# Kernel optimization log

Hardware: AMD Instinct MI355X
Metric: run time of the kernel (lower is better)

## Reference

```python
import math
import jax, jax.numpy as jnp
import numpy as np

D_MODEL = 768
NUM_HEADS = 12
NUM_KV_HEADS = 12
FEATURE_DIM = 16
HEAD_DIM = D_MODEL // NUM_KV_HEADS  # 64
EPS = 1e-12
R2 = math.sqrt(2.0)
RD = math.sqrt(FEATURE_DIM)      # sqrt(d)
RRD = math.sqrt(RD)              # d**0.25


def taylor_exp(x):
    """2nd-order Taylor feature map. x: [b,h,l,f] -> [b,h,l,1+f+f^2]."""
    b, h, l, f = x.shape
    x2 = (x[..., :, None] * x[..., None, :]).reshape(b, h, l, f * f) / R2
    ones = jnp.ones((b, h, l, 1), dtype=x.dtype)
    return jnp.concatenate([ones, x / RRD, x2 / RD], axis=-1)


def setup_inputs() -> dict:
    key = jax.random.key(0)
    k0, k1, k2, k3, k4 = jax.random.split(key, 5)
    B, L = 1, 512
    hidden_states = jax.random.normal(k0, (B, L, D_MODEL), dtype=jnp.float32)
    s = 0.02
    Wq = jax.random.normal(k1, (FEATURE_DIM * NUM_HEADS, D_MODEL), dtype=jnp.float32) * s
    Wk = jax.random.normal(k2, (FEATURE_DIM * NUM_KV_HEADS, D_MODEL), dtype=jnp.float32) * s
    Wv = jax.random.normal(k3, (NUM_KV_HEADS * HEAD_DIM, D_MODEL), dtype=jnp.float32) * s
    Wo = jax.random.normal(k4, (D_MODEL, NUM_HEADS * HEAD_DIM), dtype=jnp.float32) * s
    return {"hidden_states": hidden_states, "Wq": Wq, "Wk": Wk, "Wv": Wv, "Wo": Wo}


def reference(hidden_states, Wq, Wk, Wv, Wo):
    b, l, _ = hidden_states.shape
    # projections (nn.Linear, no bias): x @ W.T
    q = (hidden_states @ Wq.T).reshape(b, l, NUM_HEADS, FEATURE_DIM).transpose(0, 2, 1, 3)
    k = (hidden_states @ Wk.T).reshape(b, l, NUM_KV_HEADS, FEATURE_DIM).transpose(0, 2, 1, 3)
    v = (hidden_states @ Wv.T).reshape(b, l, NUM_KV_HEADS, HEAD_DIM).transpose(0, 2, 1, 3)
    q = taylor_exp(q)  # [b,h,l,D], D = 273
    k = taylor_exp(k)
    # causal linear attention: state S_t = sum_{s<=t} v_s phi(k_s)^T
    kv = k[..., None, :] * v[..., :, None]          # [b,h,l,d,D]
    kv = jnp.cumsum(kv, axis=2)
    num = jnp.einsum('bhlD,bhldD->bhld', q, kv)     # [b,h,l,d]
    den = jnp.einsum('bhlD,bhlD->bhl', q, jnp.cumsum(k, axis=2)) + EPS
    y = num / den[..., None]
    y = y.transpose(0, 2, 1, 3).reshape(b, l, NUM_HEADS * HEAD_DIM)
    return y @ Wo.T
```

## Files before the change

### kernel.cpp

```cpp
#include <hip/hip_runtime.h>

typedef short bf16x8 __attribute__((ext_vector_type(8)));
typedef float f32x4 __attribute__((ext_vector_type(4)));

__device__ __forceinline__ unsigned short f2bf(float f) {
  union { float f; unsigned int u; } v; v.f = f;
  unsigned int r = v.u + 0x7FFFu + ((v.u >> 16) & 1u);
  return (unsigned short)(r >> 16);
}

__global__ __launch_bounds__(256) void prep(
    const float* __restrict__ hs, const float* __restrict__ Wq,
    const float* __restrict__ Wk, const float* __restrict__ Wv,
    const float* __restrict__ Wo, unsigned short* __restrict__ hsb,
    unsigned short* __restrict__ Wqkvb, unsigned short* __restrict__ Wob,
    float* __restrict__ numAcc) {
  int b = blockIdx.x;
  const float* src; unsigned short* dst; int base;
  if (b < 384)       { src = hs; dst = hsb;            base = b * 1024; }
  else if (b < 528)  { src = Wq; dst = Wqkvb;          base = (b - 384) * 1024; }
  else if (b < 672)  { src = Wk; dst = Wqkvb + 147456; base = (b - 528) * 1024; }
  else if (b < 1248) { src = Wv; dst = Wqkvb + 294912; base = (b - 672) * 1024; }
  else if (b < 1824) { src = Wo; dst = Wob;            base = (b - 1248) * 1024; }
  else {
    int i = (b - 1824) * 256 + threadIdx.x;
    ((float4*)numAcc)[i] = make_float4(0.f, 0.f, 0.f, 0.f);
    return;
  }
  int i = base + threadIdx.x * 4;
  float4 x = *(const float4*)&src[i];
  ushort4 o;
  o.x = f2bf(x.x); o.y = f2bf(x.y); o.z = f2bf(x.z); o.w = f2bf(x.w);
  *(ushort4*)&dst[i] = o;
}

__global__ __launch_bounds__(256) void gemm_qkv(
    const unsigned short* __restrict__ A, const unsigned short* __restrict__ B,
    unsigned short* __restrict__ QKb, unsigned short* __restrict__ Vt) {
  __shared__ f32x4 part[4][4][64];
  const int tid = threadIdx.x;
  const int w = tid >> 6, lane = tid & 63;
  const int lm = lane & 15, quad = lane >> 4;
  const int mt = blockIdx.y * 32;
  const int n0 = blockIdx.x * 32;
  const int kw = w * 192;
  const unsigned short* a_ptr = A + (mt + lm) * 768 + kw + quad * 8;
  const unsigned short* b_ptr = B + (n0 + lm) * 768 + kw + quad * 8;
  f32x4 acc[4] = {{0.f,0.f,0.f,0.f},{0.f,0.f,0.f,0.f},{0.f,0.f,0.f,0.f},{0.f,0.f,0.f,0.f}};
#pragma unroll
  for (int kb = 0; kb < 192; kb += 32) {
    bf16x8 a0 = *(const bf16x8*)(a_ptr + kb);
    bf16x8 a1 = *(const bf16x8*)(a_ptr + 16 * 768 + kb);
    bf16x8 b0 = *(const bf16x8*)(b_ptr + kb);
    bf16x8 b1 = *(const bf16x8*)(b_ptr + 16 * 768 + kb);
    acc[0] = __builtin_amdgcn_mfma_f32_16x16x32_bf16(a0, b0, acc[0], 0, 0, 0);
    acc[1] = __builtin_amdgcn_mfma_f32_16x16x32_bf16(a0, b1, acc[1], 0, 0, 0);
    acc[2] = __builtin_amdgcn_mfma_f32_16x16x32_bf16(a1, b0, acc[2], 0, 0, 0);
    acc[3] = __builtin_amdgcn_mfma_f32_16x16x32_bf16(a1, b1, acc[3], 0, 0, 0);
  }
#pragma unroll
  for (int s = 0; s < 4; ++s) part[w][s][lane] = acc[s];
  __syncthreads();
  {
    const int m = mt + (w >> 1) * 16;
    const int n = n0 + (w & 1) * 16;
    f32x4 s = part[0][w][lane] + part[1][w][lane] + part[2][w][lane] + part[3][w][lane];
    if (n < 384) {
#pragma unroll
      for (int r = 0; r < 4; ++r)
        QKb[(m + quad * 4 + r) * 384 + n + lm] = f2bf(s[r]);
    } else {
      ushort4 o;
      o.x = f2bf(s[0]); o.y = f2bf(s[1]); o.z = f2bf(s[2]); o.w = f2bf(s[3]);
      *(ushort4*)&Vt[(n - 384 + lm) * 512 + m + quad * 4] = o;
    }
  }
}

__global__ __launch_bounds__(256) void attn(
    const unsigned short* __restrict__ QKb, const unsigned short* __restrict__ Vt,
    float* __restrict__ numAcc, float* __restrict__ denAcc) {
  int p = blockIdx.x;
  const int h = blockIdx.y, tid = threadIdx.x;
  int c = 0;
  while (p >= c + 1) { p -= c + 1; ++c; }
  const int sb = p;
  const int t0 = c * 64, s0 = sb * 64;
  __shared__ __align__(16) unsigned short scl[64 * 72];
  const int w = tid >> 6, lane = tid & 63;
  const int lm = lane & 15, quad = lane >> 4;
  bf16x8 aq = {0, 0, 0, 0, 0, 0, 0, 0};
  if (quad < 2)
    aq = *(const bf16x8*)&QKb[(t0 + w * 16 + lm) * 384 + h * 16 + quad * 8];
  f32x4 qk[4];
#pragma unroll
  for (int sbt = 0; sbt < 4; ++sbt) {
    bf16x8 bk = {0, 0, 0, 0, 0, 0, 0, 0};
    if (quad < 2)
      bk = *(const bf16x8*)&QKb[(s0 + sbt * 16 + lm) * 384 + 192 + h * 16 + quad * 8];
    f32x4 z = {0.f, 0.f, 0.f, 0.f};
    qk[sbt] = __builtin_amdgcn_mfma_f32_16x16x32_bf16(aq, bk, z, 0, 0, 0);
  }
  float dsum[4] = {0.f, 0.f, 0.f, 0.f};
#pragma unroll
  for (int sbt = 0; sbt < 4; ++sbt) {
#pragma unroll
    for (int r = 0; r < 4; ++r) {
      const int tl = w * 16 + quad * 4 + r;
      const int sl = sbt * 16 + lm;
      float x = qk[sbt][r];
      float val = (s0 + sl <= t0 + tl) ? 1.f + 0.25f * x + 0.03125f * x * x : 0.f;
      dsum[r] += val;
      scl[tl * 72 + sl] = f2bf(val);
    }
  }
  f32x4 av[4] = {{0.f,0.f,0.f,0.f},{0.f,0.f,0.f,0.f},{0.f,0.f,0.f,0.f},{0.f,0.f,0.f,0.f}};
  const unsigned short* vbase = Vt + (h * 64 + lm) * 512;
#pragma unroll
  for (int kb = 0; kb < 2; ++kb) {
    bf16x8 a = *(const bf16x8*)&scl[(w * 16 + lm) * 72 + kb * 32 + quad * 8];
#pragma unroll
    for (int dt = 0; dt < 4; ++dt) {
      bf16x8 b = *(const bf16x8*)&vbase[dt * 16 * 512 + s0 + kb * 32 + quad * 8];
      av[dt] = __builtin_amdgcn_mfma_f32_16x16x32_bf16(a, b, av[dt], 0, 0, 0);
    }
  }
#pragma unroll
  for (int r = 0; r < 4; ++r) {
    float v = dsum[r];
    v += __shfl_xor(v, 1); v += __shfl_xor(v, 2);
    v += __shfl_xor(v, 4); v += __shfl_xor(v, 8);
    if (lm == 0) atomicAdd(&denAcc[(t0 + w * 16 + quad * 4 + r) * 12 + h], v);
  }
#pragma unroll
  for (int dt = 0; dt < 4; ++dt)
#pragma unroll
    for (int r = 0; r < 4; ++r)
      atomicAdd(&numAcc[(t0 + w * 16 + quad * 4 + r) * 768 + h * 64 + dt * 16 + lm],
                av[dt][r]);
}

__global__ __launch_bounds__(256) void gemm_out(
    const float* __restrict__ numAcc, const float* __restrict__ denAcc,
    const unsigned short* __restrict__ Wob, float* __restrict__ out) {
  __shared__ f32x4 part[4][4][64];
  const int tid = threadIdx.x;
  const int w = tid >> 6, lane = tid & 63;
  const int lm = lane & 15, quad = lane >> 4;
  const int mt = blockIdx.y * 32;
  const int n0 = blockIdx.x * 32;
  const int ta = mt + lm, tb = mt + 16 + lm;
  const int kw = w * 192;
  f32x4 acc[4] = {{0.f,0.f,0.f,0.f},{0.f,0.f,0.f,0.f},{0.f,0.f,0.f,0.f},{0.f,0.f,0.f,0.f}};
#pragma unroll
  for (int kb = 0; kb < 192; kb += 32) {
    const int k0 = kw + kb + quad * 8;
    const int hh = k0 >> 6;
    float inv0 = 1.f / (denAcc[ta * 12 + hh] + 1e-12f);
    float inv1 = 1.f / (denAcc[tb * 12 + hh] + 1e-12f);
    float4 x0 = *(const float4*)&numAcc[ta * 768 + k0];
    float4 x1 = *(const float4*)&numAcc[ta * 768 + k0 + 4];
    float4 y0 = *(const float4*)&numAcc[tb * 768 + k0];
    float4 y1 = *(const float4*)&numAcc[tb * 768 + k0 + 4];
    bf16x8 a0, a1;
    a0[0] = f2bf(x0.x * inv0); a0[1] = f2bf(x0.y * inv0);
    a0[2] = f2bf(x0.z * inv0); a0[3] = f2bf(x0.w * inv0);
    a0[4] = f2bf(x1.x * inv0); a0[5] = f2bf(x1.y * inv0);
    a0[6] = f2bf(x1.z * inv0); a0[7] = f2bf(x1.w * inv0);
    a1[0] = f2bf(y0.x * inv1); a1[1] = f2bf(y0.y * inv1);
    a1[2] = f2bf(y0.z * inv1); a1[3] = f2bf(y0.w * inv1);
    a1[4] = f2bf(y1.x * inv1); a1[5] = f2bf(y1.y * inv1);
    a1[6] = f2bf(y1.z * inv1); a1[7] = f2bf(y1.w * inv1);
    bf16x8 b0 = *(const bf16x8*)&Wob[(n0 + lm) * 768 + k0];
    bf16x8 b1 = *(const bf16x8*)&Wob[(n0 + 16 + lm) * 768 + k0];
    acc[0] = __builtin_amdgcn_mfma_f32_16x16x32_bf16(a0, b0, acc[0], 0, 0, 0);
    acc[1] = __builtin_amdgcn_mfma_f32_16x16x32_bf16(a0, b1, acc[1], 0, 0, 0);
    acc[2] = __builtin_amdgcn_mfma_f32_16x16x32_bf16(a1, b0, acc[2], 0, 0, 0);
    acc[3] = __builtin_amdgcn_mfma_f32_16x16x32_bf16(a1, b1, acc[3], 0, 0, 0);
  }
#pragma unroll
  for (int s = 0; s < 4; ++s) part[w][s][lane] = acc[s];
  __syncthreads();
  {
    const int m = mt + (w >> 1) * 16;
    const int n = n0 + (w & 1) * 16;
    f32x4 s = part[0][w][lane] + part[1][w][lane] + part[2][w][lane] + part[3][w][lane];
#pragma unroll
    for (int r = 0; r < 4; ++r)
      out[(m + quad * 4 + r) * 768 + n + lm] = s[r];
  }
}

extern "C" void kernel_launch(void* const* d_in, const int* in_sizes, int n_in,
                              void* d_out, int out_size, void* d_ws, size_t ws_size,
                              hipStream_t stream) {
  const float* hs = (const float*)d_in[0];
  const float* Wq = (const float*)d_in[1];
  const float* Wk = (const float*)d_in[2];
  const float* Wv = (const float*)d_in[3];
  const float* Wo = (const float*)d_in[4];
  float* out = (float*)d_out;
  float* ws = (float*)d_ws;

  float* numAcc = ws;
  float* denAcc = ws + 393216;
  unsigned short* hsb   = (unsigned short*)(ws + 399360);
  unsigned short* Wqkvb = hsb + 393216;
  unsigned short* Wob   = Wqkvb + 884736;
  unsigned short* QKb   = Wob + 589824;
  unsigned short* Vt    = QKb + 196608;

  prep<<<dim3(2214), 256, 0, stream>>>(hs, Wq, Wk, Wv, Wo, hsb, Wqkvb, Wob, numAcc);
  gemm_qkv<<<dim3(36, 16), 256, 0, stream>>>(hsb, Wqkvb, QKb, Vt);
  attn<<<dim3(36, 12), 256, 0, stream>>>(QKb, Vt, numAcc, denAcc);
  gemm_out<<<dim3(24, 16), 256, 0, stream>>>(numAcc, denAcc, Wob, out);
}
```

Before: 103.9 us.

## Restructure causal attention to split key blocks across waves and drop atomics

The attention kernel changes from one block per (query chunk, key chunk) pair with atomic accumulation to one block per (query chunk, head, 16-row quarter). The four waves split the key chunks between them and reduce through shared memory, then write numerator and denominator with plain stores. This removes the zero-init pass over numAcc in prep and the contention from global atomics. The cost is a serial loop over key chunks per block, so load across blocks is uneven for later query chunks, and a few waves sit idle when there are fewer than four key chunks.

```diff
diff --git a/kernel.cpp b/kernel.cpp
--- a/kernel.cpp
+++ b/kernel.cpp
@@ -13,20 +13,14 @@
     const float* __restrict__ hs, const float* __restrict__ Wq,
     const float* __restrict__ Wk, const float* __restrict__ Wv,
     const float* __restrict__ Wo, unsigned short* __restrict__ hsb,
-    unsigned short* __restrict__ Wqkvb, unsigned short* __restrict__ Wob,
-    float* __restrict__ numAcc) {
+    unsigned short* __restrict__ Wqkvb, unsigned short* __restrict__ Wob) {
   int b = blockIdx.x;
   const float* src; unsigned short* dst; int base;
   if (b < 384)       { src = hs; dst = hsb;            base = b * 1024; }
   else if (b < 528)  { src = Wq; dst = Wqkvb;          base = (b - 384) * 1024; }
   else if (b < 672)  { src = Wk; dst = Wqkvb + 147456; base = (b - 528) * 1024; }
   else if (b < 1248) { src = Wv; dst = Wqkvb + 294912; base = (b - 672) * 1024; }
-  else if (b < 1824) { src = Wo; dst = Wob;            base = (b - 1248) * 1024; }
-  else {
-    int i = (b - 1824) * 256 + threadIdx.x;
-    ((float4*)numAcc)[i] = make_float4(0.f, 0.f, 0.f, 0.f);
-    return;
-  }
+  else               { src = Wo; dst = Wob;            base = (b - 1248) * 1024; }
   int i = base + threadIdx.x * 4;
   float4 x = *(const float4*)&src[i];
   ushort4 o;
@@ -80,49 +74,52 @@
 __global__ __launch_bounds__(256) void attn(
     const unsigned short* __restrict__ QKb, const unsigned short* __restrict__ Vt,
     float* __restrict__ numAcc, float* __restrict__ denAcc) {
-  int p = blockIdx.x;
-  const int h = blockIdx.y, tid = threadIdx.x;
-  int c = 0;
-  while (p >= c + 1) { p -= c + 1; ++c; }
-  const int sb = p;
-  const int t0 = c * 64, s0 = sb * 64;
-  __shared__ __align__(16) unsigned short scl[64 * 72];
+  const int c = blockIdx.x, h = blockIdx.y, tq = blockIdx.z;
+  const int tid = threadIdx.x;
   const int w = tid >> 6, lane = tid & 63;
   const int lm = lane & 15, quad = lane >> 4;
+  const int t0 = c * 64, tbase = t0 + tq * 16;
+  __shared__ __align__(16) unsigned short scl[4][16 * 72];
+  __shared__ __align__(16) f32x4 partAV[4][4][64];
+  __shared__ float denb[4][16];
   bf16x8 aq = {0, 0, 0, 0, 0, 0, 0, 0};
   if (quad < 2)
-    aq = *(const bf16x8*)&QKb[(t0 + w * 16 + lm) * 384 + h * 16 + quad * 8];
-  f32x4 qk[4];
-#pragma unroll
-  for (int sbt = 0; sbt < 4; ++sbt) {
-    bf16x8 bk = {0, 0, 0, 0, 0, 0, 0, 0};
-    if (quad < 2)
-      bk = *(const bf16x8*)&QKb[(s0 + sbt * 16 + lm) * 384 + 192 + h * 16 + quad * 8];
-    f32x4 z = {0.f, 0.f, 0.f, 0.f};
-    qk[sbt] = __builtin_amdgcn_mfma_f32_16x16x32_bf16(aq, bk, z, 0, 0, 0);
-  }
+    aq = *(const bf16x8*)&QKb[(tbase + lm) * 384 + h * 16 + quad * 8];
+  f32x4 av[4] = {{0.f,0.f,0.f,0.f},{0.f,0.f,0.f,0.f},{0.f,0.f,0.f,0.f},{0.f,0.f,0.f,0.f}};
   float dsum[4] = {0.f, 0.f, 0.f, 0.f};
-#pragma unroll
-  for (int sbt = 0; sbt < 4; ++sbt) {
-#pragma unroll
-    for (int r = 0; r < 4; ++r) {
-      const int tl = w * 16 + quad * 4 + r;
-      const int sl = sbt * 16 + lm;
-      float x = qk[sbt][r];
-      float val = (s0 + sl <= t0 + tl) ? 1.f + 0.25f * x + 0.03125f * x * x : 0.f;
-      dsum[r] += val;
-      scl[tl * 72 + sl] = f2bf(val);
-    }
-  }
-  f32x4 av[4] = {{0.f,0.f,0.f,0.f},{0.f,0.f,0.f,0.f},{0.f,0.f,0.f,0.f},{0.f,0.f,0.f,0.f}};
   const unsigned short* vbase = Vt + (h * 64 + lm) * 512;
-#pragma unroll
-  for (int kb = 0; kb < 2; ++kb) {
-    bf16x8 a = *(const bf16x8*)&scl[(w * 16 + lm) * 72 + kb * 32 + quad * 8];
-#pragma unroll
-    for (int dt = 0; dt < 4; ++dt) {
-      bf16x8 b = *(const bf16x8*)&vbase[dt * 16 * 512 + s0 + kb * 32 + quad * 8];
-      av[dt] = __builtin_amdgcn_mfma_f32_16x16x32_bf16(a, b, av[dt], 0, 0, 0);
+  unsigned short* sw = &scl[w][0];
+  for (int sb = w; sb <= c; sb += 4) {
+    const int s0 = sb * 64;
+    f32x4 qk[4];
+#pragma unroll
+    for (int sbt = 0; sbt < 4; ++sbt) {
+      bf16x8 bk = {0, 0, 0, 0, 0, 0, 0, 0};
+      if (quad < 2)
+        bk = *(const bf16x8*)&QKb[(s0 + sbt * 16 + lm) * 384 + 192 + h * 16 + quad * 8];
+      f32x4 z = {0.f, 0.f, 0.f, 0.f};
+      qk[sbt] = __builtin_amdgcn_mfma_f32_16x16x32_bf16(aq, bk, z, 0, 0, 0);
+    }
+#pragma unroll
+    for (int sbt = 0; sbt < 4; ++sbt) {
+#pragma unroll
+      for (int r = 0; r < 4; ++r) {
+        const int tl = tbase + quad * 4 + r;
+        const int sl = sbt * 16 + lm;
+        float x = qk[sbt][r];
+        float val = (s0 + sl <= tl) ? 1.f + 0.25f * x + 0.03125f * x * x : 0.f;
+        dsum[r] += val;
+        sw[(quad * 4 + r) * 72 + sl] = f2bf(val);
+      }
+    }
+#pragma unroll
+    for (int kb = 0; kb < 2; ++kb) {
+      bf16x8 a = *(const bf16x8*)&sw[lm * 72 + kb * 32 + quad * 8];
+#pragma unroll
+      for (int dt = 0; dt < 4; ++dt) {
+        bf16x8 b = *(const bf16x8*)&vbase[dt * 16 * 512 + s0 + kb * 32 + quad * 8];
+        av[dt] = __builtin_amdgcn_mfma_f32_16x16x32_bf16(a, b, av[dt], 0, 0, 0);
+      }
     }
   }
 #pragma unroll
@@ -130,14 +127,21 @@
     float v = dsum[r];
     v += __shfl_xor(v, 1); v += __shfl_xor(v, 2);
     v += __shfl_xor(v, 4); v += __shfl_xor(v, 8);
-    if (lm == 0) atomicAdd(&denAcc[(t0 + w * 16 + quad * 4 + r) * 12 + h], v);
-  }
-#pragma unroll
-  for (int dt = 0; dt < 4; ++dt)
+    if (lm == 0) denb[w][quad * 4 + r] = v;
+  }
+#pragma unroll
+  for (int dt = 0; dt < 4; ++dt) partAV[w][dt][lane] = av[dt];
+  __syncthreads();
+  if (tid < 16)
+    denAcc[(tbase + tid) * 12 + h] =
+        denb[0][tid] + denb[1][tid] + denb[2][tid] + denb[3][tid];
+  {
+    f32x4 s = partAV[0][w][lane] + partAV[1][w][lane] +
+              partAV[2][w][lane] + partAV[3][w][lane];
 #pragma unroll
     for (int r = 0; r < 4; ++r)
-      atomicAdd(&numAcc[(t0 + w * 16 + quad * 4 + r) * 768 + h * 64 + dt * 16 + lm],
-                av[dt][r]);
+      numAcc[(tbase + quad * 4 + r) * 768 + h * 64 + w * 16 + lm] = s[r];
+  }
 }
 
 __global__ __launch_bounds__(256) void gemm_out(
@@ -210,8 +214,8 @@
   unsigned short* QKb   = Wob + 589824;
   unsigned short* Vt    = QKb + 196608;
 
-  prep<<<dim3(2214), 256, 0, stream>>>(hs, Wq, Wk, Wv, Wo, hsb, Wqkvb, Wob, numAcc);
+  prep<<<dim3(1824), 256, 0, stream>>>(hs, Wq, Wk, Wv, Wo, hsb, Wqkvb, Wob);
   gemm_qkv<<<dim3(36, 16), 256, 0, stream>>>(hsb, Wqkvb, QKb, Vt);
-  attn<<<dim3(36, 12), 256, 0, stream>>>(QKb, Vt, numAcc, denAcc);
+  attn<<<dim3(8, 12, 4), 256, 0, stream>>>(QKb, Vt, numAcc, denAcc);
   gemm_out<<<dim3(24, 16), 256, 0, stream>>>(numAcc, denAcc, Wob, out);
 }
```

After: 97.63 us. 6.0% less time.
